# Kernel optimization log

Hardware: AMD Instinct MI355X
Metric: run time of the kernel (lower is better)

The kernel has to match this reference:

```python
import jax, jax.numpy as jnp
import numpy as np

LEAF = 32
N = 262144          # num_nodes, power of 2
NLEV = 8            # HODLR levels
RANK = 16           # off-diagonal low-rank
NNZ = 1310720       # ~5 nnz per row


def setup_inputs() -> dict:
    key = jax.random.key(0)
    ks = jax.random.split(key, 24)
    inp = {}
    inp["leaf_blocks"] = jax.random.normal(ks[0], (1, N // LEAF, LEAF, LEAF), jnp.float32) * 0.1
    for l in range(NLEV):
        inp[f"u{l}"] = jax.random.normal(ks[1 + 2 * l], (1, N, RANK), jnp.float32) * 0.05
        inp[f"v{l}"] = jax.random.normal(ks[2 + 2 * l], (1, N, RANK), jnp.float32) * 0.05
    inp["A_indices"] = jax.random.randint(ks[17], (2, NNZ), 0, N, dtype=jnp.int32).astype(jnp.int64)
    inp["A_values"] = jax.random.normal(ks[18], (NNZ,), jnp.float32)
    inp["z"] = jax.random.normal(ks[19], (1, N, 1), jnp.float32)
    inp["num_nodes"] = N
    return inp


def apply_hodlr(leaf_blocks, factors, x, leaf_size=LEAF):
    # x: [B, n, 1]; leaf_blocks: [B, n/leaf, leaf, leaf]
    B, n, _ = x.shape
    nb = n // leaf_size
    xb = x.reshape(B, nb, leaf_size, 1)
    L = leaf_blocks
    # y = L @ (L^T @ x) + 1e-4 * x  per leaf block
    yb = jnp.matmul(L, jnp.matmul(jnp.swapaxes(L, -1, -2), xb)) + xb * 1e-4
    y = yb.reshape(B, n, 1)
    for li, (u, v) in enumerate(factors):
        num_splits = 2 ** (li + 1)
        bs = n // num_splits
        if bs == 0:
            continue
        npair = num_splits // 2
        vl = npair * 2 * bs  # == n for power-of-2 n
        xv = x[:, :vl].reshape(B, npair, 2, bs, 1)
        uv = u[:, :vl].reshape(B, npair, 2, bs, -1)
        vv = v[:, :vl].reshape(B, npair, 2, bs, -1)
        xL, xR = xv[:, :, 0], xv[:, :, 1]
        uL, uR = uv[:, :, 0], uv[:, :, 1]
        vL, vR = vv[:, :, 0], vv[:, :, 1]
        # cross-block low-rank updates: y_L += U_L (V_R^T x_R), y_R += U_R (V_L^T x_L)
        yL = jnp.matmul(uL, jnp.matmul(jnp.swapaxes(vR, -1, -2), xR))
        yR = jnp.matmul(uR, jnp.matmul(jnp.swapaxes(vL, -1, -2), xL))
        upd = jnp.stack([yL, yR], axis=2).reshape(B, vl, 1)
        if vl < n:
            upd = jnp.pad(upd, ((0, 0), (0, n - vl), (0, 0)))
        y = y + upd
    return y


def reference(leaf_blocks, u0, v0, u1, v1, u2, v2, u3, v3, u4, v4, u5, v5, u6, v6, u7, v7,
              A_indices, A_values, z, num_nodes):
    factors = [(u0, v0), (u1, v1), (u2, v2), (u3, v3),
               (u4, v4), (u5, v5), (u6, v6), (u7, v7)]
    w = apply_hodlr(leaf_blocks, factors, z)           # [1, N, 1]
    w_flat = w[0, :, 0]                                 # [N]
    rows, cols = A_indices[0], A_indices[1]
    # sparse COO matvec: y[r] = sum_k A_values[k] * w[cols[k]] over rows
    y_flat = jax.ops.segment_sum(A_values * w_flat[cols], rows, num_segments=num_nodes)
    y = y_flat.reshape(1, num_nodes, 1)
    return jnp.mean((y - z) ** 2)
```

## Files before the change

kernel.cpp:

```cpp
#include <hip/hip_runtime.h>

#define NN 262144
#define RANK 16
#define NNZ_K 1310720
#define NB 640
#define BPB 2048
#define NBKT 256
#define RPB 1024

struct P8 { const float* p[8]; };

__global__ __launch_bounds__(512) void k_levels_t(P8 v, const float* __restrict__ z,
                                                  float* __restrict__ part) {
    __shared__ float zl[512];
    __shared__ float red[8][8][16];
    const int tid  = threadIdx.x;
    const int base = blockIdx.x * 512;

    zl[tid] = z[base + tid];
    __syncthreads();

    const int q = tid & 3;
    const int e = tid >> 2;

    float4 acc[8];
#pragma unroll
    for (int l = 0; l < 8; ++l) acc[l] = make_float4(0.f, 0.f, 0.f, 0.f);

#pragma unroll
    for (int it = 0; it < 4; ++it) {
        const int jloc = it * 128 + e;
        const size_t j = (size_t)(base + jloc);
        const float zz = zl[jloc];
        float4 vv[8];
#pragma unroll
        for (int l = 0; l < 8; ++l)
            vv[l] = *(const float4*)(v.p[l] + j * RANK + q * 4);
#pragma unroll
        for (int l = 0; l < 8; ++l) {
            acc[l].x += vv[l].x * zz;
            acc[l].y += vv[l].y * zz;
            acc[l].z += vv[l].z * zz;
            acc[l].w += vv[l].w * zz;
        }
    }

    const int lane = tid & 63;
    const int wv   = tid >> 6;
#pragma unroll
    for (int l = 0; l < 8; ++l) {
        float4 a = acc[l];
#pragma unroll
        for (int m = 4; m <= 32; m <<= 1) {
            a.x += __shfl_xor(a.x, m);
            a.y += __shfl_xor(a.y, m);
            a.z += __shfl_xor(a.z, m);
            a.w += __shfl_xor(a.w, m);
        }
        if (lane < 4) *(float4*)&red[l][wv][lane * 4] = a;
    }
    __syncthreads();

    if (tid < 128) {
        const int l = tid >> 4;
        const int r = tid & 15;
        float s = 0.f;
#pragma unroll
        for (int k = 0; k < 8; ++k) s += red[l][k][r];
        part[(l * 512 + blockIdx.x) * 16 + r] = s;
    }
}

__global__ __launch_bounds__(64) void k_reduce_t(const float* __restrict__ part,
                                                 float* __restrict__ tg,
                                                 float* __restrict__ loss) {
    const int b = blockIdx.x;
    if (b == 0 && threadIdx.x == 0) loss[0] = 0.f;
    const int t = b + 2;
    const int l = 30 - __clz(t);
    const int h = t - (2 << l);
    const int cnt = 256 >> l;
    const int c0  = h * cnt;
    const int r = threadIdx.x & 15;
    const int g = threadIdx.x >> 4;

    float s = 0.f;
    for (int c = c0 + g; c < c0 + cnt; c += 4)
        s += part[(l * 512 + c) * 16 + r];

    __shared__ float red[64];
    red[threadIdx.x] = s;
    __syncthreads();
    if (threadIdx.x < 16)
        tg[((2 << l) - 2 + h) * 16 + r] = red[r] + red[16 + r] + red[32 + r] + red[48 + r];
}

__global__ __launch_bounds__(256) void k_leaf(const float* __restrict__ leaf,
                                              const float* __restrict__ z,
                                              float* __restrict__ w) {
    const int tid = threadIdx.x;
    const int l6  = tid & 63;
    const int b   = blockIdx.x * 4 + (tid >> 6);
    const int r   = l6 >> 1;
    const int ch  = l6 & 1;

    const float* Lb = leaf + (size_t)b * 1024 + r * 32 + ch * 16;
    const float4 L0 = ((const float4*)Lb)[0];
    const float4 L1 = ((const float4*)Lb)[1];
    const float4 L2 = ((const float4*)Lb)[2];
    const float4 L3 = ((const float4*)Lb)[3];

    const float zl = z[b * 32 + (l6 & 31)];
    const float xr = __shfl(zl, r);

    float4 t0 = make_float4(L0.x * xr, L0.y * xr, L0.z * xr, L0.w * xr);
    float4 t1 = make_float4(L1.x * xr, L1.y * xr, L1.z * xr, L1.w * xr);
    float4 t2 = make_float4(L2.x * xr, L2.y * xr, L2.z * xr, L2.w * xr);
    float4 t3 = make_float4(L3.x * xr, L3.y * xr, L3.z * xr, L3.w * xr);

#pragma unroll
    for (int m = 2; m <= 32; m <<= 1) {
        t0.x += __shfl_xor(t0.x, m); t0.y += __shfl_xor(t0.y, m);
        t0.z += __shfl_xor(t0.z, m); t0.w += __shfl_xor(t0.w, m);
        t1.x += __shfl_xor(t1.x, m); t1.y += __shfl_xor(t1.y, m);
        t1.z += __shfl_xor(t1.z, m); t1.w += __shfl_xor(t1.w, m);
        t2.x += __shfl_xor(t2.x, m); t2.y += __shfl_xor(t2.y, m);
        t2.z += __shfl_xor(t2.z, m); t2.w += __shfl_xor(t2.w, m);
        t3.x += __shfl_xor(t3.x, m); t3.y += __shfl_xor(t3.y, m);
        t3.z += __shfl_xor(t3.z, m); t3.w += __shfl_xor(t3.w, m);
    }

    float yp = L0.x * t0.x + L0.y * t0.y + L0.z * t0.z + L0.w * t0.w
             + L1.x * t1.x + L1.y * t1.y + L1.z * t1.z + L1.w * t1.w
             + L2.x * t2.x + L2.y * t2.y + L2.z * t2.z + L2.w * t2.w
             + L3.x * t3.x + L3.y * t3.y + L3.z * t3.z + L3.w * t3.w;
    yp += __shfl_xor(yp, 1);

    const float w0 = yp + 1e-4f * xr;

    const float out = __shfl(w0, (l6 & 31) * 2);
    if (l6 < 32) w[(size_t)b * 32 + l6] = out;
}

__global__ __launch_bounds__(128) void k_uacc(P8 u,
                                              const float* __restrict__ tg,
                                              float* __restrict__ w,
                                              float* __restrict__ y) {
    __shared__ float tl[8][16];
    const int tid  = threadIdx.x;
    const int base = blockIdx.x * 128;
    const size_t i = (size_t)(base + tid);

    {
        const int l = tid >> 4;
        const int r = tid & 15;
        const int h = base >> (17 - l);
        tl[l][r] = tg[(((2 << l) - 2) + (h ^ 1)) * 16 + r];
    }

    float4 a[16];
#pragma unroll
    for (int l = 0; l < 4; ++l) {
        const float4* up = (const float4*)(u.p[l] + i * RANK);
#pragma unroll
        for (int k = 0; k < 4; ++k) a[l * 4 + k] = up[k];
    }
    const float accw = w[i];
    __syncthreads();

    float accs[8];
#pragma unroll
    for (int l = 0; l < 4; ++l) {
        const float4 t0 = *(const float4*)&tl[l][0];
        const float4 t1 = *(const float4*)&tl[l][4];
        const float4 t2 = *(const float4*)&tl[l][8];
        const float4 t3 = *(const float4*)&tl[l][12];
        accs[l] = a[l*4+0].x * t0.x + a[l*4+0].y * t0.y + a[l*4+0].z * t0.z + a[l*4+0].w * t0.w
                + a[l*4+1].x * t1.x + a[l*4+1].y * t1.y + a[l*4+1].z * t1.z + a[l*4+1].w * t1.w
                + a[l*4+2].x * t2.x + a[l*4+2].y * t2.y + a[l*4+2].z * t2.z + a[l*4+2].w * t2.w
                + a[l*4+3].x * t3.x + a[l*4+3].y * t3.y + a[l*4+3].z * t3.z + a[l*4+3].w * t3.w;
    }

#pragma unroll
    for (int l = 0; l < 4; ++l) {
        const float4* up = (const float4*)(u.p[l + 4] + i * RANK);
#pragma unroll
        for (int k = 0; k < 4; ++k) a[l * 4 + k] = up[k];
    }
#pragma unroll
    for (int l = 0; l < 4; ++l) {
        const float4 t0 = *(const float4*)&tl[l + 4][0];
        const float4 t1 = *(const float4*)&tl[l + 4][4];
        const float4 t2 = *(const float4*)&tl[l + 4][8];
        const float4 t3 = *(const float4*)&tl[l + 4][12];
        accs[l + 4] = a[l*4+0].x * t0.x + a[l*4+0].y * t0.y + a[l*4+0].z * t0.z + a[l*4+0].w * t0.w
                    + a[l*4+1].x * t1.x + a[l*4+1].y * t1.y + a[l*4+1].z * t1.z + a[l*4+1].w * t1.w
                    + a[l*4+2].x * t2.x + a[l*4+2].y * t2.y + a[l*4+2].z * t2.z + a[l*4+2].w * t2.w
                    + a[l*4+3].x * t3.x + a[l*4+3].y * t3.y + a[l*4+3].z * t3.z + a[l*4+3].w * t3.w;
    }

    w[i] = accw + ((accs[0] + accs[1]) + (accs[2] + accs[3]))
                + ((accs[4] + accs[5]) + (accs[6] + accs[7]));
    if (y) y[i] = 0.f;
}

__global__ __launch_bounds__(512) void k_bin(const int* __restrict__ idx,
                                             const float* __restrict__ vals,
                                             const float* __restrict__ w,
                                             unsigned long long* __restrict__ gpairs,
                                             int* __restrict__ gdesc) {
    __shared__ unsigned long long pairs[BPB];
    __shared__ int hist[NBKT];
    __shared__ int scan[NBKT];
    __shared__ int cursor[NBKT];

    const int t  = threadIdx.x;
    const int bl = blockIdx.x;
    const int base = bl * BPB;

    if (t < NBKT) hist[t] = 0;
    __syncthreads();

    int   rows[4];
    float pv[4];
    {
        const int k = base + t * 4;
        const int4   r4 = *(const int4*)(idx + k);
        const int4   c4 = *(const int4*)(idx + NNZ_K + k);
        const float4 v4 = *(const float4*)(vals + k);
        rows[0] = r4.x; pv[0] = v4.x * w[c4.x];
        rows[1] = r4.y; pv[1] = v4.y * w[c4.y];
        rows[2] = r4.z; pv[2] = v4.z * w[c4.z];
        rows[3] = r4.w; pv[3] = v4.w * w[c4.w];
        atomicAdd(&hist[r4.x >> 10], 1);
        atomicAdd(&hist[r4.y >> 10], 1);
        atomicAdd(&hist[r4.z >> 10], 1);
        atomicAdd(&hist[r4.w >> 10], 1);
    }
    __syncthreads();

    int cnt = 0;
    if (t < NBKT) { cnt = hist[t]; scan[t] = cnt; }
    __syncthreads();
    for (int off = 1; off < NBKT; off <<= 1) {
        int add = 0;
        if (t >= off && t < NBKT) add = scan[t - off];
        __syncthreads();
        if (t < NBKT) scan[t] += add;
        __syncthreads();
    }
    if (t < NBKT) {
        const int st = scan[t] - cnt;
        gdesc[t * NB + bl] = st | (cnt << 16);
        cursor[t] = st;
    }
    __syncthreads();

#pragma unroll
    for (int i = 0; i < 4; ++i) {
        const int b   = rows[i] >> 10;
        const int pos = atomicAdd(&cursor[b], 1);
        pairs[pos] = ((unsigned long long)__float_as_uint(pv[i]) << 32) | (unsigned)rows[i];
    }
    __syncthreads();

    const ulonglong2* ps = (const ulonglong2*)pairs;
    ulonglong2*       pd = (ulonglong2*)(gpairs + (size_t)bl * BPB);
#pragma unroll
    for (int i = 0; i < 2; ++i)
        pd[i * 512 + t] = ps[i * 512 + t];
}

__global__ __launch_bounds__(1024) void k_accum(const unsigned long long* __restrict__ gpairs,
                                                const int* __restrict__ gdesc,
                                                const float* __restrict__ z,
                                                float* __restrict__ loss) {
    __shared__ float acc[RPB];
    __shared__ float red[16];
    const int t = threadIdx.x;
    const int b = blockIdx.x;
    acc[t] = 0.f;
    __syncthreads();

    if (t < NB) {
        const int d  = gdesc[b * NB + t];
        const int st = d & 0xffff;
        const int c  = d >> 16;
        const unsigned long long* p = gpairs + (size_t)t * BPB + st;
        for (int j = 0; j < c; ++j) {
            const unsigned long long pr = p[j];
            atomicAdd(&acc[(int)(pr & 1023u)], __uint_as_float((unsigned)(pr >> 32)));
        }
    }
    __syncthreads();

    const float d = acc[t] - z[b * RPB + t];
    float s = d * d;
#pragma unroll
    for (int m = 32; m >= 1; m >>= 1) s += __shfl_down(s, m);
    if ((t & 63) == 0) red[t >> 6] = s;
    __syncthreads();
    if (t == 0) {
        float tt = 0.f;
#pragma unroll
        for (int i = 0; i < 16; ++i) tt += red[i];
        atomicAdd(loss, tt);
    }
}

__global__ __launch_bounds__(256) void k_spmv(const int* __restrict__ idx,
                                              const float* __restrict__ vals,
                                              const float* __restrict__ w,
                                              float* __restrict__ y) {
    const int k = (blockIdx.x * 256 + threadIdx.x) * 4;
    const int4   r4 = *(const int4*)(idx + k);
    const int4   c4 = *(const int4*)(idx + NNZ_K + k);
    const float4 v4 = *(const float4*)(vals + k);
    atomicAdd(&y[r4.x], v4.x * w[c4.x]);
    atomicAdd(&y[r4.y], v4.y * w[c4.y]);
    atomicAdd(&y[r4.z], v4.z * w[c4.z]);
    atomicAdd(&y[r4.w], v4.w * w[c4.w]);
}

__global__ __launch_bounds__(256) void k_loss(const float* __restrict__ y,
                                              const float* __restrict__ z,
                                              float* __restrict__ loss) {
    const int i = blockIdx.x * 256 + threadIdx.x;
    const float4 a = ((const float4*)y)[i];
    const float4 b = ((const float4*)z)[i];
    const float dx = a.x - b.x, dy = a.y - b.y, dz = a.z - b.z, dw = a.w - b.w;
    float s = dx * dx + dy * dy + dz * dz + dw * dw;
#pragma unroll
    for (int m = 32; m >= 1; m >>= 1) s += __shfl_down(s, m);
    __shared__ float r4s[4];
    const int lane = threadIdx.x & 63, wv = threadIdx.x >> 6;
    if (lane == 0) r4s[wv] = s;
    __syncthreads();
    if (threadIdx.x == 0) atomicAdd(loss, r4s[0] + r4s[1] + r4s[2] + r4s[3]);
}

__global__ void k_fin(const float* __restrict__ loss, float* __restrict__ out) {
    out[0] = loss[0] * (1.0f / (float)NN);
}

extern "C" void kernel_launch(void* const* d_in, const int* in_sizes, int n_in,
                              void* d_out, int out_size, void* d_ws, size_t ws_size,
                              hipStream_t stream) {
    const float* leaf = (const float*)d_in[0];
    P8 u, v;
    for (int l = 0; l < 8; ++l) {
        u.p[l] = (const float*)d_in[1 + 2 * l];
        v.p[l] = (const float*)d_in[2 + 2 * l];
    }
    const int*   Aidx  = (const int*)d_in[17];
    const float* Avals = (const float*)d_in[18];
    const float* z     = (const float*)d_in[19];

    float* ws   = (float*)d_ws;
    float* part  = ws;
    float* tg    = ws + 65536;
    float* loss  = ws + 73728;
    float* w     = ws + 73792;
    int*   gdesc = (int*)(ws + 335936);
    unsigned long long* gpairs = (unsigned long long*)(ws + 499776);
    const size_t need_main = (size_t)(499776 + (size_t)NB * BPB * 2) * 4;

    k_levels_t<<<NN / 512, 512, 0, stream>>>(v, z, part);
    k_reduce_t<<<510, 64, 0, stream>>>(part, tg, loss);
    k_leaf    <<<NN / 128, 256, 0, stream>>>(leaf, z, w);

    if (ws_size >= need_main) {
        k_uacc <<<NN / 128, 128, 0, stream>>>(u, tg, w, nullptr);
        k_bin  <<<NB, 512, 0, stream>>>(Aidx, Avals, w, gpairs, gdesc);
        k_accum<<<NBKT, 1024, 0, stream>>>(gpairs, gdesc, z, loss);
    } else {
        float* y = ws + 335936;
        k_uacc <<<NN / 128, 128, 0, stream>>>(u, tg, w, y);
        k_spmv <<<NNZ_K / 1024, 256, 0, stream>>>(Aidx, Avals, w, y);
        k_loss <<<NN / 1024, 256, 0, stream>>>(y, z, loss);
    }
    k_fin<<<1, 1, 0, stream>>>(loss, (float*)d_out);
}
```

Baseline: 362.5 us.

## Fuse leaf and U-accumulation kernels, shrink level blocks, rebalance binning

Merges the leaf-block matvec and the low-rank U accumulation into one kernel, so w is computed in shared memory and written once instead of being written and reread. The V^T z reduction kernel now uses smaller 256-thread blocks over 2048 chunks with an occupancy hint, and the second-stage reduction uses wider blocks. The COO binning uses 512 blocks of 640 threads, and accumulation assigns two threads per source bin. These changes add more partial sums and more workspace, and shift load balance across several kernels.

```diff
diff --git a/kernel.cpp b/kernel.cpp
--- a/kernel.cpp
+++ b/kernel.cpp
@@ -3,208 +3,203 @@
 #define NN 262144
 #define RANK 16
 #define NNZ_K 1310720
-#define NB 640
-#define BPB 2048
+#define NB 512
+#define BPB 2560
 #define NBKT 256
 #define RPB 1024
+#define NCH 2048
 
 struct P8 { const float* p[8]; };
 
-__global__ __launch_bounds__(512) void k_levels_t(P8 v, const float* __restrict__ z,
-                                                  float* __restrict__ part) {
-    __shared__ float zl[512];
-    __shared__ float red[8][8][16];
+__global__ __launch_bounds__(256, 6) void k_levels_t(P8 v, const float* __restrict__ z,
+                                                     float* __restrict__ part) {
+    __shared__ float red[8][4][16];
     const int tid  = threadIdx.x;
-    const int base = blockIdx.x * 512;
-
-    zl[tid] = z[base + tid];
-    __syncthreads();
-
-    const int q = tid & 3;
-    const int e = tid >> 2;
-
-    float4 acc[8];
-#pragma unroll
-    for (int l = 0; l < 8; ++l) acc[l] = make_float4(0.f, 0.f, 0.f, 0.f);
-
-#pragma unroll
-    for (int it = 0; it < 4; ++it) {
-        const int jloc = it * 128 + e;
-        const size_t j = (size_t)(base + jloc);
-        const float zz = zl[jloc];
-        float4 vv[8];
-#pragma unroll
-        for (int l = 0; l < 8; ++l)
-            vv[l] = *(const float4*)(v.p[l] + j * RANK + q * 4);
-#pragma unroll
-        for (int l = 0; l < 8; ++l) {
-            acc[l].x += vv[l].x * zz;
-            acc[l].y += vv[l].y * zz;
-            acc[l].z += vv[l].z * zz;
-            acc[l].w += vv[l].w * zz;
-        }
-    }
-
+    const int base = blockIdx.x * 128;
+    const int q    = tid & 3;
+    const int e    = tid >> 2;
     const int lane = tid & 63;
     const int wv   = tid >> 6;
-#pragma unroll
-    for (int l = 0; l < 8; ++l) {
-        float4 a = acc[l];
-#pragma unroll
-        for (int m = 4; m <= 32; m <<= 1) {
-            a.x += __shfl_xor(a.x, m);
-            a.y += __shfl_xor(a.y, m);
-            a.z += __shfl_xor(a.z, m);
-            a.w += __shfl_xor(a.w, m);
-        }
-        if (lane < 4) *(float4*)&red[l][wv][lane * 4] = a;
+
+#pragma unroll
+    for (int g = 0; g < 2; ++g) {
+        float4 acc[4];
+#pragma unroll
+        for (int l = 0; l < 4; ++l) acc[l] = make_float4(0.f, 0.f, 0.f, 0.f);
+
+#pragma unroll
+        for (int it = 0; it < 2; ++it) {
+            const int jl = it * 64 + e;
+            const size_t j = (size_t)(base + jl);
+            const float zz = z[j];
+            float4 vv[4];
+#pragma unroll
+            for (int l = 0; l < 4; ++l)
+                vv[l] = *(const float4*)(v.p[g * 4 + l] + j * RANK + q * 4);
+#pragma unroll
+            for (int l = 0; l < 4; ++l) {
+                acc[l].x += vv[l].x * zz;
+                acc[l].y += vv[l].y * zz;
+                acc[l].z += vv[l].z * zz;
+                acc[l].w += vv[l].w * zz;
+            }
+        }
+
+#pragma unroll
+        for (int l = 0; l < 4; ++l) {
+            float4 a = acc[l];
+#pragma unroll
+            for (int m = 4; m <= 32; m <<= 1) {
+                a.x += __shfl_xor(a.x, m);
+                a.y += __shfl_xor(a.y, m);
+                a.z += __shfl_xor(a.z, m);
+                a.w += __shfl_xor(a.w, m);
+            }
+            if (lane < 4) *(float4*)&red[g * 4 + l][wv][lane * 4] = a;
+        }
     }
     __syncthreads();
 
     if (tid < 128) {
         const int l = tid >> 4;
         const int r = tid & 15;
-        float s = 0.f;
-#pragma unroll
-        for (int k = 0; k < 8; ++k) s += red[l][k][r];
-        part[(l * 512 + blockIdx.x) * 16 + r] = s;
-    }
-}
-
-__global__ __launch_bounds__(64) void k_reduce_t(const float* __restrict__ part,
-                                                 float* __restrict__ tg,
-                                                 float* __restrict__ loss) {
+        const float s = red[l][0][r] + red[l][1][r] + red[l][2][r] + red[l][3][r];
+        part[(l * NCH + blockIdx.x) * 16 + r] = s;
+    }
+}
+
+__global__ __launch_bounds__(256) void k_reduce_t(const float* __restrict__ part,
+                                                  float* __restrict__ tg,
+                                                  float* __restrict__ loss) {
     const int b = blockIdx.x;
     if (b == 0 && threadIdx.x == 0) loss[0] = 0.f;
     const int t = b + 2;
     const int l = 30 - __clz(t);
     const int h = t - (2 << l);
-    const int cnt = 256 >> l;
+    const int cnt = 1024 >> l;
     const int c0  = h * cnt;
     const int r = threadIdx.x & 15;
     const int g = threadIdx.x >> 4;
 
     float s = 0.f;
-    for (int c = c0 + g; c < c0 + cnt; c += 4)
-        s += part[(l * 512 + c) * 16 + r];
-
-    __shared__ float red[64];
+    for (int c = c0 + g; c < c0 + cnt; c += 16)
+        s += part[(l * NCH + c) * 16 + r];
+
+    __shared__ float red[256];
     red[threadIdx.x] = s;
     __syncthreads();
-    if (threadIdx.x < 16)
-        tg[((2 << l) - 2 + h) * 16 + r] = red[r] + red[16 + r] + red[32 + r] + red[48 + r];
-}
-
-__global__ __launch_bounds__(256) void k_leaf(const float* __restrict__ leaf,
+    if (threadIdx.x < 16) {
+        float ss = 0.f;
+#pragma unroll
+        for (int k = 0; k < 16; ++k) ss += red[k * 16 + r];
+        tg[((2 << l) - 2 + h) * 16 + r] = ss;
+    }
+}
+
+__global__ __launch_bounds__(256, 6) void k_w(const float* __restrict__ leaf, P8 u,
                                               const float* __restrict__ z,
-                                              float* __restrict__ w) {
-    const int tid = threadIdx.x;
-    const int l6  = tid & 63;
-    const int b   = blockIdx.x * 4 + (tid >> 6);
-    const int r   = l6 >> 1;
-    const int ch  = l6 & 1;
-
-    const float* Lb = leaf + (size_t)b * 1024 + r * 32 + ch * 16;
-    const float4 L0 = ((const float4*)Lb)[0];
-    const float4 L1 = ((const float4*)Lb)[1];
-    const float4 L2 = ((const float4*)Lb)[2];
-    const float4 L3 = ((const float4*)Lb)[3];
-
-    const float zl = z[b * 32 + (l6 & 31)];
-    const float xr = __shfl(zl, r);
-
-    float4 t0 = make_float4(L0.x * xr, L0.y * xr, L0.z * xr, L0.w * xr);
-    float4 t1 = make_float4(L1.x * xr, L1.y * xr, L1.z * xr, L1.w * xr);
-    float4 t2 = make_float4(L2.x * xr, L2.y * xr, L2.z * xr, L2.w * xr);
-    float4 t3 = make_float4(L3.x * xr, L3.y * xr, L3.z * xr, L3.w * xr);
-
-#pragma unroll
-    for (int m = 2; m <= 32; m <<= 1) {
-        t0.x += __shfl_xor(t0.x, m); t0.y += __shfl_xor(t0.y, m);
-        t0.z += __shfl_xor(t0.z, m); t0.w += __shfl_xor(t0.w, m);
-        t1.x += __shfl_xor(t1.x, m); t1.y += __shfl_xor(t1.y, m);
-        t1.z += __shfl_xor(t1.z, m); t1.w += __shfl_xor(t1.w, m);
-        t2.x += __shfl_xor(t2.x, m); t2.y += __shfl_xor(t2.y, m);
-        t2.z += __shfl_xor(t2.z, m); t2.w += __shfl_xor(t2.w, m);
-        t3.x += __shfl_xor(t3.x, m); t3.y += __shfl_xor(t3.y, m);
-        t3.z += __shfl_xor(t3.z, m); t3.w += __shfl_xor(t3.w, m);
-    }
-
-    float yp = L0.x * t0.x + L0.y * t0.y + L0.z * t0.z + L0.w * t0.w
-             + L1.x * t1.x + L1.y * t1.y + L1.z * t1.z + L1.w * t1.w
-             + L2.x * t2.x + L2.y * t2.y + L2.z * t2.z + L2.w * t2.w
-             + L3.x * t3.x + L3.y * t3.y + L3.z * t3.z + L3.w * t3.w;
-    yp += __shfl_xor(yp, 1);
-
-    const float w0 = yp + 1e-4f * xr;
-
-    const float out = __shfl(w0, (l6 & 31) * 2);
-    if (l6 < 32) w[(size_t)b * 32 + l6] = out;
-}
-
-__global__ __launch_bounds__(128) void k_uacc(P8 u,
                                               const float* __restrict__ tg,
                                               float* __restrict__ w,
                                               float* __restrict__ y) {
+    __shared__ float wl[128];
+    __shared__ float pb[128];
     __shared__ float tl[8][16];
+
     const int tid  = threadIdx.x;
     const int base = blockIdx.x * 128;
-    const size_t i = (size_t)(base + tid);
-
-    {
+
+    if (tid < 128) {
         const int l = tid >> 4;
         const int r = tid & 15;
         const int h = base >> (17 - l);
         tl[l][r] = tg[(((2 << l) - 2) + (h ^ 1)) * 16 + r];
     }
 
-    float4 a[16];
-#pragma unroll
-    for (int l = 0; l < 4; ++l) {
-        const float4* up = (const float4*)(u.p[l] + i * RANK);
-#pragma unroll
-        for (int k = 0; k < 4; ++k) a[l * 4 + k] = up[k];
-    }
-    const float accw = w[i];
-    __syncthreads();
-
-    float accs[8];
-#pragma unroll
-    for (int l = 0; l < 4; ++l) {
-        const float4 t0 = *(const float4*)&tl[l][0];
-        const float4 t1 = *(const float4*)&tl[l][4];
-        const float4 t2 = *(const float4*)&tl[l][8];
-        const float4 t3 = *(const float4*)&tl[l][12];
-        accs[l] = a[l*4+0].x * t0.x + a[l*4+0].y * t0.y + a[l*4+0].z * t0.z + a[l*4+0].w * t0.w
-                + a[l*4+1].x * t1.x + a[l*4+1].y * t1.y + a[l*4+1].z * t1.z + a[l*4+1].w * t1.w
-                + a[l*4+2].x * t2.x + a[l*4+2].y * t2.y + a[l*4+2].z * t2.z + a[l*4+2].w * t2.w
-                + a[l*4+3].x * t3.x + a[l*4+3].y * t3.y + a[l*4+3].z * t3.z + a[l*4+3].w * t3.w;
-    }
-
-#pragma unroll
-    for (int l = 0; l < 4; ++l) {
-        const float4* up = (const float4*)(u.p[l + 4] + i * RANK);
-#pragma unroll
-        for (int k = 0; k < 4; ++k) a[l * 4 + k] = up[k];
-    }
-#pragma unroll
-    for (int l = 0; l < 4; ++l) {
-        const float4 t0 = *(const float4*)&tl[l + 4][0];
-        const float4 t1 = *(const float4*)&tl[l + 4][4];
-        const float4 t2 = *(const float4*)&tl[l + 4][8];
-        const float4 t3 = *(const float4*)&tl[l + 4][12];
-        accs[l + 4] = a[l*4+0].x * t0.x + a[l*4+0].y * t0.y + a[l*4+0].z * t0.z + a[l*4+0].w * t0.w
-                    + a[l*4+1].x * t1.x + a[l*4+1].y * t1.y + a[l*4+1].z * t1.z + a[l*4+1].w * t1.w
-                    + a[l*4+2].x * t2.x + a[l*4+2].y * t2.y + a[l*4+2].z * t2.z + a[l*4+2].w * t2.w
-                    + a[l*4+3].x * t3.x + a[l*4+3].y * t3.y + a[l*4+3].z * t3.z + a[l*4+3].w * t3.w;
-    }
-
-    w[i] = accw + ((accs[0] + accs[1]) + (accs[2] + accs[3]))
-                + ((accs[4] + accs[5]) + (accs[6] + accs[7]));
-    if (y) y[i] = 0.f;
-}
-
-__global__ __launch_bounds__(512) void k_bin(const int* __restrict__ idx,
+    {
+        const int l6 = tid & 63;
+        const int wv = tid >> 6;
+        const int b  = blockIdx.x * 4 + wv;
+        const int r  = l6 >> 1;
+
+        const float* Lb = leaf + (size_t)b * 1024 + r * 32 + (l6 & 1) * 16;
+        const float4 L0 = ((const float4*)Lb)[0];
+        const float4 L1 = ((const float4*)Lb)[1];
+        const float4 L2 = ((const float4*)Lb)[2];
+        const float4 L3 = ((const float4*)Lb)[3];
+
+        const float zl = z[b * 32 + (l6 & 31)];
+        const float xr = __shfl(zl, r);
+
+        float4 t0 = make_float4(L0.x * xr, L0.y * xr, L0.z * xr, L0.w * xr);
+        float4 t1 = make_float4(L1.x * xr, L1.y * xr, L1.z * xr, L1.w * xr);
+        float4 t2 = make_float4(L2.x * xr, L2.y * xr, L2.z * xr, L2.w * xr);
+        float4 t3 = make_float4(L3.x * xr, L3.y * xr, L3.z * xr, L3.w * xr);
+
+#pragma unroll
+        for (int m = 2; m <= 32; m <<= 1) {
+            t0.x += __shfl_xor(t0.x, m); t0.y += __shfl_xor(t0.y, m);
+            t0.z += __shfl_xor(t0.z, m); t0.w += __shfl_xor(t0.w, m);
+            t1.x += __shfl_xor(t1.x, m); t1.y += __shfl_xor(t1.y, m);
+            t1.z += __shfl_xor(t1.z, m); t1.w += __shfl_xor(t1.w, m);
+            t2.x += __shfl_xor(t2.x, m); t2.y += __shfl_xor(t2.y, m);
+            t2.z += __shfl_xor(t2.z, m); t2.w += __shfl_xor(t2.w, m);
+            t3.x += __shfl_xor(t3.x, m); t3.y += __shfl_xor(t3.y, m);
+            t3.z += __shfl_xor(t3.z, m); t3.w += __shfl_xor(t3.w, m);
+        }
+
+        float yp = L0.x * t0.x + L0.y * t0.y + L0.z * t0.z + L0.w * t0.w
+                 + L1.x * t1.x + L1.y * t1.y + L1.z * t1.z + L1.w * t1.w
+                 + L2.x * t2.x + L2.y * t2.y + L2.z * t2.z + L2.w * t2.w
+                 + L3.x * t3.x + L3.y * t3.y + L3.z * t3.z + L3.w * t3.w;
+        yp += __shfl_xor(yp, 1);
+
+        const float w0  = yp + 1e-4f * xr;
+        const float out = __shfl(w0, (l6 & 31) * 2);
+        if (l6 < 32) wl[wv * 32 + l6] = out;
+    }
+    __syncthreads();
+
+    const int half = tid >> 7;
+    const int e    = tid & 127;
+    const size_t i = (size_t)(base + e);
+    const int l0   = half * 4;
+
+    float accs[4];
+#pragma unroll
+    for (int lp = 0; lp < 2; ++lp) {
+        const int l = l0 + lp * 2;
+        float4 a[8];
+        {
+            const float4* up0 = (const float4*)(u.p[l] + i * RANK);
+            const float4* up1 = (const float4*)(u.p[l + 1] + i * RANK);
+#pragma unroll
+            for (int k = 0; k < 4; ++k) a[k]     = up0[k];
+#pragma unroll
+            for (int k = 0; k < 4; ++k) a[4 + k] = up1[k];
+        }
+#pragma unroll
+        for (int s = 0; s < 2; ++s) {
+            const float4 t0 = *(const float4*)&tl[l + s][0];
+            const float4 t1 = *(const float4*)&tl[l + s][4];
+            const float4 t2 = *(const float4*)&tl[l + s][8];
+            const float4 t3 = *(const float4*)&tl[l + s][12];
+            const float4* av = &a[s * 4];
+            accs[lp * 2 + s] = av[0].x * t0.x + av[0].y * t0.y + av[0].z * t0.z + av[0].w * t0.w
+                             + av[1].x * t1.x + av[1].y * t1.y + av[1].z * t1.z + av[1].w * t1.w
+                             + av[2].x * t2.x + av[2].y * t2.y + av[2].z * t2.z + av[2].w * t2.w
+                             + av[3].x * t3.x + av[3].y * t3.y + av[3].z * t3.z + av[3].w * t3.w;
+        }
+    }
+    const float sum = (accs[0] + accs[1]) + (accs[2] + accs[3]);
+    if (half) pb[e] = sum;
+    __syncthreads();
+    if (!half) {
+        w[i] = wl[e] + sum + pb[e];
+        if (y) y[i] = 0.f;
+    }
+}
+
+__global__ __launch_bounds__(640) void k_bin(const int* __restrict__ idx,
                                              const float* __restrict__ vals,
                                              const float* __restrict__ w,
                                              unsigned long long* __restrict__ gpairs,
@@ -268,7 +263,7 @@
     ulonglong2*       pd = (ulonglong2*)(gpairs + (size_t)bl * BPB);
 #pragma unroll
     for (int i = 0; i < 2; ++i)
-        pd[i * 512 + t] = ps[i * 512 + t];
+        pd[i * 640 + t] = ps[i * 640 + t];
 }
 
 __global__ __launch_bounds__(1024) void k_accum(const unsigned long long* __restrict__ gpairs,
@@ -282,12 +277,14 @@
     acc[t] = 0.f;
     __syncthreads();
 
-    if (t < NB) {
-        const int d  = gdesc[b * NB + t];
+    {
+        const int s  = t >> 1;
+        const int h  = t & 1;
+        const int d  = gdesc[b * NB + s];
         const int st = d & 0xffff;
         const int c  = d >> 16;
-        const unsigned long long* p = gpairs + (size_t)t * BPB + st;
-        for (int j = 0; j < c; ++j) {
+        const unsigned long long* p = gpairs + (size_t)s * BPB + st;
+        for (int j = h; j < c; j += 2) {
             const unsigned long long pr = p[j];
             atomicAdd(&acc[(int)(pr & 1023u)], __uint_as_float((unsigned)(pr >> 32)));
         }
@@ -358,24 +355,23 @@
 
     float* ws   = (float*)d_ws;
     float* part  = ws;
-    float* tg    = ws + 65536;
-    float* loss  = ws + 73728;
-    float* w     = ws + 73792;
-    int*   gdesc = (int*)(ws + 335936);
-    unsigned long long* gpairs = (unsigned long long*)(ws + 499776);
-    const size_t need_main = (size_t)(499776 + (size_t)NB * BPB * 2) * 4;
-
-    k_levels_t<<<NN / 512, 512, 0, stream>>>(v, z, part);
-    k_reduce_t<<<510, 64, 0, stream>>>(part, tg, loss);
-    k_leaf    <<<NN / 128, 256, 0, stream>>>(leaf, z, w);
+    float* tg    = ws + 262144;
+    float* loss  = ws + 270336;
+    float* w     = ws + 270400;
+    int*   gdesc = (int*)(ws + 532544);
+    unsigned long long* gpairs = (unsigned long long*)(ws + 663616);
+    const size_t need_main = (size_t)(663616 + (size_t)NB * BPB * 2) * 4;
+
+    k_levels_t<<<NCH, 256, 0, stream>>>(v, z, part);
+    k_reduce_t<<<510, 256, 0, stream>>>(part, tg, loss);
 
     if (ws_size >= need_main) {
-        k_uacc <<<NN / 128, 128, 0, stream>>>(u, tg, w, nullptr);
-        k_bin  <<<NB, 512, 0, stream>>>(Aidx, Avals, w, gpairs, gdesc);
+        k_w    <<<NN / 128, 256, 0, stream>>>(leaf, u, z, tg, w, nullptr);
+        k_bin  <<<NB, 640, 0, stream>>>(Aidx, Avals, w, gpairs, gdesc);
         k_accum<<<NBKT, 1024, 0, stream>>>(gpairs, gdesc, z, loss);
     } else {
-        float* y = ws + 335936;
-        k_uacc <<<NN / 128, 128, 0, stream>>>(u, tg, w, y);
+        float* y = ws + 532544;
+        k_w    <<<NN / 128, 256, 0, stream>>>(leaf, u, z, tg, w, y);
         k_spmv <<<NNZ_K / 1024, 256, 0, stream>>>(Aidx, Avals, w, y);
         k_loss <<<NN / 1024, 256, 0, stream>>>(y, z, loss);
     }
```

After: 355.0 us. 1.02x faster.
